# Optimization experiments

Measured on AMD Instinct MI355X. Metric: run time of the kernel, lower is better.

## Reference

```python
import jax, jax.numpy as jnp
import numpy as np

H = 256          # hidden_dim
B = 64           # molecules
M = 64           # atoms per molecule (equal-size molecules)
N = B * M        # total nodes
NE = 119         # element classes
NB = 5           # bond classes
EPS = 1e-5
OFF_I, OFF_J = np.where(~np.eye(M, dtype=bool))  # static off-diagonal pair order (i-major, j!=i)


def _gelu(x):
    return jax.nn.gelu(x, approximate=False)


def _ln(x, g, b):
    mu = jnp.mean(x, axis=-1, keepdims=True)
    var = jnp.mean((x - mu) ** 2, axis=-1, keepdims=True)
    return (x - mu) * jax.lax.rsqrt(var + EPS) * g + b


def _mlp(x, W1, b1, g, bn, W2, b2, W3, b3):
    x = _gelu(x @ W1 + b1)
    x = _ln(x, g, bn)
    x = _gelu(x @ W2 + b2)
    return x @ W3 + b3


def setup_inputs():
    key = jax.random.key(0)
    ks = jax.random.split(key, 16)
    s = 0.02
    def lin(k, fi, fo):
        return jax.random.normal(k, (fi, fo), jnp.float32) * s
    inp = {}
    inp["h"] = jax.random.normal(ks[0], (N, H), jnp.float32)
    inp["pos"] = jax.random.normal(ks[1], (N, 3), jnp.float32) * 3.0
    inp["edge_index"] = jax.random.randint(ks[2], (2, N * 8), 0, N)
    inp["batch"] = jnp.repeat(jnp.arange(B), M)
    # atom_predictor params
    inp["aW1"] = lin(ks[3], H, H); inp["ab1"] = jnp.zeros((H,))
    inp["ag"] = jnp.ones((H,)); inp["abn"] = jnp.zeros((H,))
    inp["aW2"] = lin(ks[4], H, H // 2); inp["ab2"] = jnp.zeros((H // 2,))
    inp["aW3"] = lin(ks[5], H // 2, NE); inp["ab3"] = jnp.zeros((NE,))
    # valency_predictor params
    inp["vW1"] = lin(ks[6], H + NE, H); inp["vb1"] = jnp.zeros((H,))
    inp["vg"] = jnp.ones((H,)); inp["vbn"] = jnp.zeros((H,))
    inp["vW2"] = lin(ks[7], H, H // 2); inp["vb2"] = jnp.zeros((H // 2,))
    inp["vW3"] = lin(ks[8], H // 2, 1); inp["vb3"] = jnp.zeros((1,))
    # bond_predictor params
    inp["bW1"] = lin(ks[9], 2 * H + 4, H); inp["bb1"] = jnp.zeros((H,))
    inp["bg"] = jnp.ones((H,)); inp["bbn"] = jnp.zeros((H,))
    inp["bW2"] = lin(ks[10], H, H // 2); inp["bb2"] = jnp.zeros((H // 2,))
    inp["bW3"] = lin(ks[11], H // 2, NB); inp["bb3"] = jnp.zeros((NB,))
    # chemical constant buffers (stand-ins for RDKit tables)
    mv = np.ones(NE, np.float32) * 4.0
    mv[[1, 9, 17, 35, 53]] = 1.0; mv[8] = 2.0; mv[7] = 3.0; mv[16] = 6.0; mv[15] = 5.0
    inp["max_valences"] = jnp.asarray(mv)
    cr = np.ones(NE, np.float32) * 1.5
    cr[1] = 0.31; cr[6] = 0.76; cr[7] = 0.71; cr[8] = 0.66; cr[9] = 0.57; cr[16] = 1.05
    inp["covalent_radii"] = jnp.asarray(cr)
    return inp


def _forward(h, pos, aW1, ab1, ag, abn, aW2, ab2, aW3, ab3,
             vW1, vb1, vg, vbn, vW2, vb2, vW3, vb3,
             bW1, bb1, bg, bbn, bW2, bb2, bW3, bb3,
             max_valences, covalent_radii):
    atom_logits = _mlp(h, aW1, ab1, ag, abn, aW2, ab2, aW3, ab3)        # [N,119]
    atom_probs = jax.nn.softmax(atom_logits, axis=-1)
    val = _mlp(jnp.concatenate([h, atom_probs], -1), vW1, vb1, vg, vbn, vW2, vb2, vW3, vb3)
    val = jax.nn.softplus(val)                                          # [N,1]
    pred = jnp.clip(jnp.argmax(atom_probs, -1), 0, 118)
    max_allowed = max_valences[pred]                                    # [N]
    # torch.min([N], [N,1]) broadcasts to [N,N] in the original -- reproduced faithfully
    valency_constrained = jnp.minimum(val[:, 0], max_allowed[:, None])  # [N,N]
    # vectorized pairwise bond prediction per molecule (equal-size molecules)
    hB = h.reshape(B, M, H)
    pB = pos.reshape(B, M, 3)
    probsB = atom_probs.reshape(B, M, NE)
    dist = jnp.linalg.norm(pB[:, :, None, :] - pB[:, None, :, :], axis=-1)  # [B,M,M]
    radii = covalent_radii[jnp.minimum(jnp.argmax(probsB, -1), 118)]        # [B,M]
    expected = radii[:, :, None] + radii[:, None, :]                        # [B,M,M]
    close = (dist < 3.0).astype(h.dtype)
    feats = jnp.concatenate([
        jnp.broadcast_to(hB[:, :, None, :], (B, M, M, H)),
        jnp.broadcast_to(hB[:, None, :, :], (B, M, M, H)),
        dist[..., None], expected[..., None],
        (dist / expected)[..., None], close[..., None],
    ], axis=-1)                                                             # [B,M,M,2H+4]
    logits = _mlp(feats, bW1, bb1, bg, bbn, bW2, bb2, bW3, bb3)             # [B,M,M,5]
    probs5 = jax.nn.softmax(logits, axis=-1)
    e0 = jnp.zeros((NB,), h.dtype).at[0].set(1.0)
    diag = jnp.eye(M, dtype=bool)[None, :, :, None]
    adjacency = jnp.where(diag, e0, probs5)                                 # [B,M,M,5]
    bond_logits = logits[:, OFF_I, OFF_J, :].reshape(B * M * (M - 1), NB)   # skip i==j, i-major order
    return (atom_logits, bond_logits, valency_constrained, adjacency)


def reference(h, pos, edge_index, batch, aW1, ab1, ag, abn, aW2, ab2, aW3, ab3,
              vW1, vb1, vg, vbn, vW2, vb2, vW3, vb3,
              bW1, bb1, bg, bbn, bW2, bb2, bW3, bb3, max_valences, covalent_radii):
    # edge_index is unused by the original forward; batch is implicit in the [B,M] layout
    return _forward(h, pos, aW1, ab1, ag, abn, aW2, ab2, aW3, ab3,
                    vW1, vb1, vg, vbn, vW2, vb2, vW3, vb3,
                    bW1, bb1, bg, bbn, bW2, bb2, bW3, bb3,
                    max_valences, covalent_radii)
```

## Files before the change

### kernel.cpp

```cpp
#include <hip/hip_runtime.h>
#include <math.h>

#define NN   4096
#define HH   256
#define NEC  119
#define NBC  5
#define NMOL 64
#define MAT  64

#define OFF_ATOM   0
#define SZ_ATOM    (4096*119)
#define OFF_BOND   487424
#define SZ_BOND    (258048*5)
#define OFF_VALM   (487424+1290240)
#define SZ_VALM    (4096*4096)
#define OFF_ADJ    (1777664+16777216)

typedef short  bf16x8 __attribute__((ext_vector_type(8)));
typedef float  f32x4  __attribute__((ext_vector_type(4)));

__device__ __forceinline__ float gelu_f(float x) {
    float z = fabsf(x) * 0.70710678118654752f;
    float t = __builtin_amdgcn_rcpf(fmaf(0.3275911f, z, 1.0f));
    float p = t * fmaf(t, fmaf(t, fmaf(t, fmaf(t, 1.061405429f, -1.453152027f),
                                       1.421413741f), -0.284496736f), 0.254829592f);
    float er = fmaf(-p, __expf(-z * z), 1.0f);
    float s = copysignf(er, x);
    return 0.5f * x * (1.f + s);
}
__device__ __forceinline__ unsigned short f2bf(float x) {
    unsigned int u = __float_as_uint(x);
    unsigned int r = (u + 0x7fffu + ((u >> 16) & 1u)) >> 16;
    return (unsigned short)r;
}

__global__ __launch_bounds__(256, 8) void k_front(
    const float* __restrict__ h,
    const float* __restrict__ aW1, const float* __restrict__ ab1,
    const float* __restrict__ ag,  const float* __restrict__ abn,
    const float* __restrict__ aW2, const float* __restrict__ ab2,
    const float* __restrict__ aW3, const float* __restrict__ ab3,
    const float* __restrict__ maxv, const float* __restrict__ covr,
    const float* __restrict__ vW1, const float* __restrict__ vb1,
    const float* __restrict__ vg,  const float* __restrict__ vbn,
    const float* __restrict__ vW2, const float* __restrict__ vb2,
    const float* __restrict__ vW3, const float* __restrict__ vb3,
    const float* __restrict__ bW1, const float* __restrict__ bb1,
    const float* __restrict__ bW2, const float* __restrict__ bW3,
    const float* __restrict__ bg,  const float* __restrict__ bbn,
    const float* __restrict__ bb2,
    float* __restrict__ logits_out,
    float* __restrict__ ma, float* __restrict__ rad, float* __restrict__ val,
    float* __restrict__ P, float* __restrict__ Q,
    short* __restrict__ W2f, short* __restrict__ W3f,
    float* __restrict__ uu, float* __restrict__ vvb)
{
    __shared__ float smem[3532];
    float (*hs)[376]   = (float(*)[376])smem;
    float (*z1)[256]   = (float(*)[256])(smem + 1504);
    float (*z2)[128]   = (float(*)[128])(smem + 2528);
    float (*llog)[120] = (float(*)[120])(smem + 3040);
    float (*redbuf)[2] = (float(*)[2])  (smem + 3520);

    const int t  = threadIdx.x;
    const int wv = t >> 6, ln = t & 63;

    if (blockIdx.x >= 1024) {
        const int pb = blockIdx.x - 1024;
        const int n0 = pb * 4;

        if (pb < 128) {
            const int id = pb * 256 + t;
            {
                const int e = id & 7, l = (id >> 3) & 63, ks = (id >> 9) & 7, ct = (id >> 12) & 7;
                const int k = ks * 32 + (l >> 4) * 8 + e;
                const int col = ct * 16 + (l & 15);
                W2f[id] = (short)f2bf(bW2[k * 128 + col]);
            }
            if (id < 2048) {
                const int e = id & 7, l = (id >> 3) & 63, ks = id >> 9;
                const int k = ks * 32 + (l >> 4) * 8 + e;
                const int col = l & 15;
                W3f[id] = (col < NBC) ? (short)f2bf(bW3[k * NBC + col]) : (short)0;
            }
        } else if (pb == 128) {
            if (t < 128) {
                float ua = 0.f, va = 0.f;
                for (int c = 0; c < 256; ++c) {
                    float w = bW2[c * 128 + t];
                    ua = fmaf(bg[c],  w, ua);
                    va = fmaf(bbn[c], w, va);
                }
                uu[t]  = ua;
                vvb[t] = va + bb2[t];
            }
        }

        float (*hq)[256] = (float(*)[256])smem;
        for (int idx = t; idx < 4 * 256; idx += 256)
            ((float*)hq)[idx] = h[(size_t)n0 * 256 + idx];
        __syncthreads();

        const int c = t;
        float accp[4], accq[4];
        float b1 = bb1[c];
        #pragma unroll
        for (int r = 0; r < 4; ++r) { accp[r] = b1; accq[r] = 0.f; }
        for (int k4 = 0; k4 < 64; ++k4) {
            const int k = k4 * 4;
            float p0 = bW1[(k + 0) * 256 + c];
            float p1 = bW1[(k + 1) * 256 + c];
            float p2 = bW1[(k + 2) * 256 + c];
            float p3 = bW1[(k + 3) * 256 + c];
            float q0 = bW1[(256 + k + 0) * 256 + c];
            float q1 = bW1[(256 + k + 1) * 256 + c];
            float q2 = bW1[(256 + k + 2) * 256 + c];
            float q3 = bW1[(256 + k + 3) * 256 + c];
            #pragma unroll
            for (int r = 0; r < 4; ++r) {
                float4 hv = *(const float4*)&hq[r][k];
                accp[r] = fmaf(hv.x, p0, accp[r]);
                accp[r] = fmaf(hv.y, p1, accp[r]);
                accp[r] = fmaf(hv.z, p2, accp[r]);
                accp[r] = fmaf(hv.w, p3, accp[r]);
                accq[r] = fmaf(hv.x, q0, accq[r]);
                accq[r] = fmaf(hv.y, q1, accq[r]);
                accq[r] = fmaf(hv.z, q2, accq[r]);
                accq[r] = fmaf(hv.w, q3, accq[r]);
            }
        }
        #pragma unroll
        for (int r = 0; r < 4; ++r) {
            P[(size_t)(n0 + r) * 256 + c] = accp[r];
            Q[(size_t)(n0 + r) * 256 + c] = accq[r];
        }
        return;
    }

    const int n0 = blockIdx.x * 4;

    for (int idx = t; idx < 4 * 256; idx += 256) {
        int r = idx >> 8, cc = idx & 255;
        hs[r][cc] = h[(size_t)(n0 + r) * 256 + cc];
    }
    if (t < 4) hs[t][375] = 0.f;
    __syncthreads();

    {
        const int c = t;
        float b1 = ab1[c];
        float acc[4];
        #pragma unroll
        for (int r = 0; r < 4; ++r) acc[r] = b1;
        for (int k4 = 0; k4 < 64; ++k4) {
            const int k = k4 * 4;
            float w0 = aW1[(k + 0) * 256 + c];
            float w1 = aW1[(k + 1) * 256 + c];
            float w2 = aW1[(k + 2) * 256 + c];
            float w3 = aW1[(k + 3) * 256 + c];
            #pragma unroll
            for (int r = 0; r < 4; ++r) {
                float4 hv = *(const float4*)&hs[r][k];
                acc[r] = fmaf(hv.x, w0, acc[r]);
                acc[r] = fmaf(hv.y, w1, acc[r]);
                acc[r] = fmaf(hv.z, w2, acc[r]);
                acc[r] = fmaf(hv.w, w3, acc[r]);
            }
        }
        #pragma unroll
        for (int r = 0; r < 4; ++r) z1[r][c] = gelu_f(acc[r]);
    }
    __syncthreads();

    {
        const int r = wv;
        float s = 0.f, s2 = 0.f;
        #pragma unroll
        for (int q = 0; q < 4; ++q) {
            float v = z1[r][ln + q * 64];
            s += v; s2 = fmaf(v, v, s2);
        }
        #pragma unroll
        for (int m = 32; m >= 1; m >>= 1) {
            s  += __shfl_xor(s,  m, 64);
            s2 += __shfl_xor(s2, m, 64);
        }
        if (ln == 0) {
            float mu  = s * (1.f / 256.f);
            float var = s2 * (1.f / 256.f) - mu * mu;
            redbuf[r][0] = mu;
            redbuf[r][1] = rsqrtf(var + 1e-5f);
        }
    }
    __syncthreads();
    {
        const int c = t;
        float g = ag[c], b = abn[c];
        #pragma unroll
        for (int r = 0; r < 4; ++r)
            z1[r][c] = (z1[r][c] - redbuf[r][0]) * redbuf[r][1] * g + b;
    }
    __syncthreads();

    {
        const int c2 = t & 127, kh = t >> 7;
        float acc2[4];
        #pragma unroll
        for (int r = 0; r < 4; ++r) acc2[r] = 0.f;
        const int kb = kh * 128;
        for (int k4 = 0; k4 < 32; ++k4) {
            const int k = kb + k4 * 4;
            float w0 = aW2[(k + 0) * 128 + c2];
            float w1 = aW2[(k + 1) * 128 + c2];
            float w2 = aW2[(k + 2) * 128 + c2];
            float w3 = aW2[(k + 3) * 128 + c2];
            #pragma unroll
            for (int r = 0; r < 4; ++r) {
                float4 zv = *(const float4*)&z1[r][k];
                acc2[r] = fmaf(zv.x, w0, acc2[r]);
                acc2[r] = fmaf(zv.y, w1, acc2[r]);
                acc2[r] = fmaf(zv.z, w2, acc2[r]);
                acc2[r] = fmaf(zv.w, w3, acc2[r]);
            }
        }
        if (kh == 1) {
            #pragma unroll
            for (int r = 0; r < 4; ++r) z2[r][c2] = acc2[r];
        }
        __syncthreads();
        if (kh == 0) {
            float b2 = ab2[c2];
            #pragma unroll
            for (int r = 0; r < 4; ++r)
                z2[r][c2] = gelu_f(acc2[r] + z2[r][c2] + b2);
        }
    }
    __syncthreads();

    if (t < NEC) {
        const int c = t;
        float b3 = ab3[c];
        float acc3[4];
        #pragma unroll
        for (int r = 0; r < 4; ++r) acc3[r] = b3;
        for (int k4 = 0; k4 < 32; ++k4) {
            const int k = k4 * 4;
            float w0 = aW3[(k + 0) * NEC + c];
            float w1 = aW3[(k + 1) * NEC + c];
            float w2 = aW3[(k + 2) * NEC + c];
            float w3 = aW3[(k + 3) * NEC + c];
            #pragma unroll
            for (int r = 0; r < 4; ++r) {
                float4 zv = *(const float4*)&z2[r][k];
                acc3[r] = fmaf(zv.x, w0, acc3[r]);
                acc3[r] = fmaf(zv.y, w1, acc3[r]);
                acc3[r] = fmaf(zv.z, w2, acc3[r]);
                acc3[r] = fmaf(zv.w, w3, acc3[r]);
            }
        }
        #pragma unroll
        for (int r = 0; r < 4; ++r) {
            llog[r][c] = acc3[r];
            logits_out[(size_t)(n0 + r) * NEC + c] = acc3[r];
        }
    }
    __syncthreads();

    {
        const int r = wv;
        float v1 = llog[r][ln];
        float v2 = (ln + 64 < NEC) ? llog[r][ln + 64] : -1e30f;
        float mx; int mi;
        if (v2 > v1) { mx = v2; mi = ln + 64; } else { mx = v1; mi = ln; }
        #pragma unroll
        for (int m = 32; m >= 1; m >>= 1) {
            float ov = __shfl_xor(mx, m, 64);
            int   oi = __shfl_xor(mi, m, 64);
            if (ov > mx || (ov == mx && oi < mi)) { mx = ov; mi = oi; }
        }
        float e1 = __expf(v1 - mx);
        float e2 = (ln + 64 < NEC) ? __expf(v2 - mx) : 0.f;
        float s = e1 + e2;
        #pragma unroll
        for (int m = 32; m >= 1; m >>= 1) s += __shfl_xor(s, m, 64);
        float inv = __builtin_amdgcn_rcpf(s);
        hs[r][256 + ln] = e1 * inv;
        if (ln + 64 < NEC) hs[r][256 + ln + 64] = e2 * inv;
        if (ln == 0) {
            ma[n0 + r]  = maxv[mi];
            rad[n0 + r] = covr[mi];
        }
    }
    __syncthreads();

    {
        const int c = t;
        float b1 = vb1[c];
        float acc[4];
        #pragma unroll
        for (int r = 0; r < 4; ++r) acc[r] = b1;
        for (int k4 = 0; k4 < 93; ++k4) {
            const int k = k4 * 4;
            float w0 = vW1[(k + 0) * 256 + c];
            float w1 = vW1[(k + 1) * 256 + c];
            float w2 = vW1[(k + 2) * 256 + c];
            float w3 = vW1[(k + 3) * 256 + c];
            #pragma unroll
            for (int r = 0; r < 4; ++r) {
                float4 hv = *(const float4*)&hs[r][k];
                acc[r] = fmaf(hv.x, w0, acc[r]);
                acc[r] = fmaf(hv.y, w1, acc[r]);
                acc[r] = fmaf(hv.z, w2, acc[r]);
                acc[r] = fmaf(hv.w, w3, acc[r]);
            }
        }
        {
            float w0 = vW1[372 * 256 + c];
            float w1 = vW1[373 * 256 + c];
            float w2 = vW1[374 * 256 + c];
            #pragma unroll
            for (int r = 0; r < 4; ++r) {
                acc[r] = fmaf(hs[r][372], w0, acc[r]);
                acc[r] = fmaf(hs[r][373], w1, acc[r]);
                acc[r] = fmaf(hs[r][374], w2, acc[r]);
            }
        }
        #pragma unroll
        for (int r = 0; r < 4; ++r) z1[r][c] = gelu_f(acc[r]);
    }
    __syncthreads();

    {
        const int r = wv;
        float s = 0.f, s2 = 0.f;
        #pragma unroll
        for (int q = 0; q < 4; ++q) {
            float v = z1[r][ln + q * 64];
            s += v; s2 = fmaf(v, v, s2);
        }
        #pragma unroll
        for (int m = 32; m >= 1; m >>= 1) {
            s  += __shfl_xor(s,  m, 64);
            s2 += __shfl_xor(s2, m, 64);
        }
        if (ln == 0) {
            float mu  = s * (1.f / 256.f);
            float var = s2 * (1.f / 256.f) - mu * mu;
            redbuf[r][0] = mu;
            redbuf[r][1] = rsqrtf(var + 1e-5f);
        }
    }
    __syncthreads();
    {
        const int c = t;
        float g = vg[c], b = vbn[c];
        #pragma unroll
        for (int r = 0; r < 4; ++r)
            z1[r][c] = (z1[r][c] - redbuf[r][0]) * redbuf[r][1] * g + b;
    }
    __syncthreads();

    {
        const int c2 = t & 127, kh = t >> 7;
        float acc2[4];
        #pragma unroll
        for (int r = 0; r < 4; ++r) acc2[r] = 0.f;
        const int kb = kh * 128;
        for (int k4 = 0; k4 < 32; ++k4) {
            const int k = kb + k4 * 4;
            float w0 = vW2[(k + 0) * 128 + c2];
            float w1 = vW2[(k + 1) * 128 + c2];
            float w2 = vW2[(k + 2) * 128 + c2];
            float w3 = vW2[(k + 3) * 128 + c2];
            #pragma unroll
            for (int r = 0; r < 4; ++r) {
                float4 zv = *(const float4*)&z1[r][k];
                acc2[r] = fmaf(zv.x, w0, acc2[r]);
                acc2[r] = fmaf(zv.y, w1, acc2[r]);
                acc2[r] = fmaf(zv.z, w2, acc2[r]);
                acc2[r] = fmaf(zv.w, w3, acc2[r]);
            }
        }
        if (kh == 1) {
            #pragma unroll
            for (int r = 0; r < 4; ++r) z2[r][c2] = acc2[r];
        }
        __syncthreads();
        if (kh == 0) {
            float b2 = vb2[c2];
            #pragma unroll
            for (int r = 0; r < 4; ++r)
                z2[r][c2] = gelu_f(acc2[r] + z2[r][c2] + b2);
        }
    }
    __syncthreads();

    {
        const int r = wv;
        float p = fmaf(z2[r][ln], vW3[ln], z2[r][ln + 64] * vW3[ln + 64]);
        #pragma unroll
        for (int m = 32; m >= 1; m >>= 1) p += __shfl_xor(p, m, 64);
        if (ln == 0) {
            float x = p + vb3[0];
            val[n0 + r] = (x > 15.f) ? x : log1pf(expf(x));
        }
    }
}

__global__ __launch_bounds__(256, 4) void k_back(
    const float* __restrict__ pos, const float* __restrict__ rad,
    const float* __restrict__ P, const float* __restrict__ Q,
    const float* __restrict__ bW1, const float* __restrict__ bg,
    const short* __restrict__ W2f, const short* __restrict__ W3f,
    const float* __restrict__ bb3,
    const float* __restrict__ uu, const float* __restrict__ vvb,
    const float* __restrict__ val, const float* __restrict__ ma,
    float* __restrict__ bond_logits, float* __restrict__ adjacency,
    float* __restrict__ valmat)
{
    __shared__ float posr[64][4];
    __shared__ float Pis[256];
    __shared__ float wst0[256], wst1[256], wst2[256], wst3[256];
    __shared__ float gams[256];
    __shared__ float us_[128], vbs[128];
    __shared__ unsigned short Ys[64 * 128];
    __shared__ float Ls[64][5];

    const int t  = threadIdx.x;

    if (blockIdx.x >= 4096) {
        const int i0 = (blockIdx.x - 4096) * 8;
        const float4* v4 = (const float4*)val;
        for (int rr = 0; rr < 8; ++rr) {
            const int i = i0 + rr;
            const float mi = ma[i];
            float4* o4 = (float4*)(valmat + (size_t)i * 4096);
            for (int j = t; j < 1024; j += 256) {
                float4 v = v4[j];
                float4 r;
                r.x = fminf(v.x, mi); r.y = fminf(v.y, mi);
                r.z = fminf(v.z, mi); r.w = fminf(v.w, mi);
                o4[j] = r;
            }
        }
        return;
    }

    const int bi = blockIdx.x;
    const int b  = bi >> 6, i = bi & 63;
    const int wv = t >> 6, ln = t & 63;
    const int lr = ln & 15, kg = ln >> 4;
    const int node0 = b * 64;
    const int j = wv * 16 + lr;

    if (t < 64) {
        int n = node0 + t;
        posr[t][0] = pos[n * 3 + 0];
        posr[t][1] = pos[n * 3 + 1];
        posr[t][2] = pos[n * 3 + 2];
        posr[t][3] = rad[n];
    }
    Pis[t]  = P[(size_t)(node0 + i) * 256 + t];
    wst0[t] = bW1[(size_t)512 * 256 + t];
    wst1[t] = bW1[(size_t)513 * 256 + t];
    wst2[t] = bW1[(size_t)514 * 256 + t];
    wst3[t] = bW1[(size_t)515 * 256 + t];
    gams[t] = bg[t];
    if (t < 128) { us_[t] = uu[t]; vbs[t] = vvb[t]; }
    __syncthreads();

    float dx = posr[i][0] - posr[j][0];
    float dy = posr[i][1] - posr[j][1];
    float dz = posr[i][2] - posr[j][2];
    float dist  = sqrtf(fmaf(dx, dx, fmaf(dy, dy, dz * dz)));
    float expd  = posr[i][3] + posr[j][3];
    float ratio = dist * __builtin_amdgcn_rcpf(expd);
    float close = (dist < 3.f) ? 1.f : 0.f;

    float s = 0.f, s2 = 0.f;
    bf16x8 afr[8];
    const float* Qrow = Q + (size_t)(node0 + j) * 256;
    #pragma unroll
    for (int ks = 0; ks < 8; ++ks) {
        const int base = ks * 32 + kg * 8;
        float4 Pa  = *(const float4*)&Pis[base],  Pb  = *(const float4*)&Pis[base + 4];
        float4 Qa  = *(const float4*)(Qrow + base), Qb = *(const float4*)(Qrow + base + 4);
        float4 w0a = *(const float4*)&wst0[base], w0b = *(const float4*)&wst0[base + 4];
        float4 w1a = *(const float4*)&wst1[base], w1b = *(const float4*)&wst1[base + 4];
        float4 w2a = *(const float4*)&wst2[base], w2b = *(const float4*)&wst2[base + 4];
        float4 w3a = *(const float4*)&wst3[base], w3b = *(const float4*)&wst3[base + 4];
        float4 ga  = *(const float4*)&gams[base], gb  = *(const float4*)&gams[base + 4];
        float g, xg;
        #define LANECH(P_, Q_, W0_, W1_, W2_, W3_, G_, EI) \
            g = P_ + Q_; g = fmaf(W0_, dist, g); g = fmaf(W1_, expd, g); \
            g = fmaf(W2_, ratio, g); g = fmaf(W3_, close, g); g = gelu_f(g); \
            s += g; s2 = fmaf(g, g, s2); xg = g * G_; afr[ks][EI] = (short)f2bf(xg);
        LANECH(Pa.x, Qa.x, w0a.x, w1a.x, w2a.x, w3a.x, ga.x, 0)
        LANECH(Pa.y, Qa.y, w0a.y, w1a.y, w2a.y, w3a.y, ga.y, 1)
        LANECH(Pa.z, Qa.z, w0a.z, w1a.z, w2a.z, w3a.z, ga.z, 2)
        LANECH(Pa.w, Qa.w, w0a.w, w1a.w, w2a.w, w3a.w, ga.w, 3)
        LANECH(Pb.x, Qb.x, w0b.x, w1b.x, w2b.x, w3b.x, gb.x, 4)
        LANECH(Pb.y, Qb.y, w0b.y, w1b.y, w2b.y, w3b.y, gb.y, 5)
        LANECH(Pb.z, Qb.z, w0b.z, w1b.z, w2b.z, w3b.z, gb.z, 6)
        LANECH(Pb.w, Qb.w, w0b.w, w1b.w, w2b.w, w3b.w, gb.w, 7)
        #undef LANECH
    }
    s  += __shfl_xor(s,  16, 64);  s  += __shfl_xor(s,  32, 64);
    s2 += __shfl_xor(s2, 16, 64);  s2 += __shfl_xor(s2, 32, 64);
    const float mu   = s * (1.f / 256.f);
    const float rstd = rsqrtf(s2 * (1.f / 256.f) - mu * mu + 1e-5f);

    f32x4 acc[8];
    #pragma unroll
    for (int ct = 0; ct < 8; ++ct) acc[ct] = (f32x4){0.f, 0.f, 0.f, 0.f};
    #pragma unroll
    for (int ks = 0; ks < 8; ++ks) {
        #pragma unroll
        for (int ct = 0; ct < 8; ++ct) {
            bf16x8 bfr = *(const bf16x8*)(W2f + (((size_t)(ct * 8 + ks)) * 64 + ln) * 8);
            acc[ct] = __builtin_amdgcn_mfma_f32_16x16x32_bf16(afr[ks], bfr, acc[ct], 0, 0, 0);
        }
    }

    float rst[4], rm[4];
    #pragma unroll
    for (int r = 0; r < 4; ++r) {
        float sr = __shfl(rstd, kg * 4 + r, 64);
        float mr = __shfl(mu,   kg * 4 + r, 64);
        rst[r] = sr; rm[r] = sr * mr;
    }
    #pragma unroll
    for (int ct = 0; ct < 8; ++ct) {
        const int col = ct * 16 + lr;
        const float ucv = us_[col], vcv = vbs[col];
        #pragma unroll
        for (int r = 0; r < 4; ++r) {
            float y = fmaf(rst[r], acc[ct][r], fmaf(-rm[r], ucv, vcv));
            y = gelu_f(y);
            const int row = wv * 16 + kg * 4 + r;
            const int chunk = col >> 3;
            const int off = row * 256 + ((chunk ^ (row & 7)) << 4) + ((col & 7) << 1);
            *(unsigned short*)((char*)Ys + off) = f2bf(y);
        }
    }

    {
        f32x4 acc3 = (f32x4){0.f, 0.f, 0.f, 0.f};
        #pragma unroll
        for (int ks = 0; ks < 4; ++ks) {
            bf16x8 bfr = *(const bf16x8*)(W3f + ((size_t)(ks * 64 + ln)) * 8);
            const int row   = wv * 16 + lr;
            const int chunk = ks * 4 + kg;
            const int off   = row * 256 + ((chunk ^ (row & 7)) << 4);
            bf16x8 afr2 = *(const bf16x8*)((char*)Ys + off);
            acc3 = __builtin_amdgcn_mfma_f32_16x16x32_bf16(afr2, bfr, acc3, 0, 0, 0);
        }
        if (lr < NBC) {
            #pragma unroll
            for (int r = 0; r < 4; ++r)
                Ls[wv * 16 + kg * 4 + r][lr] = acc3[r];
        }
    }

    const size_t adjbase  = (size_t)bi * 64 * 5;
    const size_t bondbase = ((size_t)b * 4032 + (size_t)i * 63) * 5;
    const float b30 = bb3[0], b31 = bb3[1], b32 = bb3[2], b33 = bb3[3], b34 = bb3[4];
    for (int u = ln; u < 80; u += 64) {
        const int jl = u / 5, o = u - jl * 5;
        const int j2 = wv * 16 + jl;
        float l0 = Ls[j2][0] + b30, l1 = Ls[j2][1] + b31, l2 = Ls[j2][2] + b32;
        float l3 = Ls[j2][3] + b33, l4 = Ls[j2][4] + b34;
        float mx = fmaxf(fmaxf(fmaxf(l0, l1), fmaxf(l2, l3)), l4);
        float e0 = __expf(l0 - mx), e1 = __expf(l1 - mx), e2 = __expf(l2 - mx);
        float e3 = __expf(l3 - mx), e4 = __expf(l4 - mx);
        float inv = __builtin_amdgcn_rcpf(e0 + e1 + e2 + e3 + e4);
        float lo = (o == 0) ? l0 : (o == 1) ? l1 : (o == 2) ? l2 : (o == 3) ? l3 : l4;
        float po = ((o == 0) ? e0 : (o == 1) ? e1 : (o == 2) ? e2 : (o == 3) ? e3 : e4) * inv;
        adjacency[adjbase + (size_t)j2 * 5 + o] = (j2 == i) ? ((o == 0) ? 1.f : 0.f) : po;
        if (j2 != i) {
            const int jj = j2 - (j2 > i ? 1 : 0);
            bond_logits[bondbase + (size_t)jj * 5 + o] = lo;
        }
    }
}

extern "C" void kernel_launch(void* const* d_in, const int* in_sizes, int n_in,
                              void* d_out, int out_size, void* d_ws, size_t ws_size,
                              hipStream_t stream)
{
    (void)in_sizes; (void)n_in; (void)out_size; (void)ws_size;
    const float* h   = (const float*)d_in[0];
    const float* pos = (const float*)d_in[1];
    const float* aW1 = (const float*)d_in[4];
    const float* ab1 = (const float*)d_in[5];
    const float* ag  = (const float*)d_in[6];
    const float* abn = (const float*)d_in[7];
    const float* aW2 = (const float*)d_in[8];
    const float* ab2 = (const float*)d_in[9];
    const float* aW3 = (const float*)d_in[10];
    const float* ab3 = (const float*)d_in[11];
    const float* vW1 = (const float*)d_in[12];
    const float* vb1 = (const float*)d_in[13];
    const float* vg  = (const float*)d_in[14];
    const float* vbn = (const float*)d_in[15];
    const float* vW2 = (const float*)d_in[16];
    const float* vb2 = (const float*)d_in[17];
    const float* vW3 = (const float*)d_in[18];
    const float* vb3 = (const float*)d_in[19];
    const float* bW1 = (const float*)d_in[20];
    const float* bb1 = (const float*)d_in[21];
    const float* bg  = (const float*)d_in[22];
    const float* bbn = (const float*)d_in[23];
    const float* bW2 = (const float*)d_in[24];
    const float* bb2 = (const float*)d_in[25];
    const float* bW3 = (const float*)d_in[26];
    const float* bb3 = (const float*)d_in[27];
    const float* mv  = (const float*)d_in[28];
    const float* cr  = (const float*)d_in[29];

    float* out = (float*)d_out;
    float* atom_logits = out + OFF_ATOM;
    float* bond_logits = out + OFF_BOND;
    float* valmat      = out + OFF_VALM;
    float* adjacency   = out + OFF_ADJ;

    float* ws    = (float*)d_ws;
    float* ma    = ws;
    float* rad   = ws + 4096;
    float* val   = ws + 8192;
    float* Pp    = ws + 12288;
    float* Qq    = ws + 1060864;
    short* W2f   = (short*)(ws + 2109440);
    short* W3f   = (short*)(ws + 2125824);
    float* uu    = ws + 2126848;
    float* vvb   = ws + 2126976;

    k_front<<<2048, 256, 0, stream>>>(h,
        aW1, ab1, ag, abn, aW2, ab2, aW3, ab3, mv, cr,
        vW1, vb1, vg, vbn, vW2, vb2, vW3, vb3,
        bW1, bb1, bW2, bW3, bg, bbn, bb2,
        atom_logits, ma, rad, val, Pp, Qq, W2f, W3f, uu, vvb);
    k_back<<<4608, 256, 0, stream>>>(pos, rad, Pp, Qq, bW1, bg,
                                     W2f, W3f, bb3, uu, vvb, val, ma,
                                     bond_logits, adjacency, valmat);
}
```

Measured before the change: 356.9 us.

## Move P/Q projection and valency MLP onto bf16 MFMA with a weight-prep kernel

Adds a k_prep kernel that converts the bond W1 (P/Q halves), valency W1/W2 and bond W2/W3 weights into bf16 MFMA fragment layouts. The front kernel now computes the P/Q node projections as 64x64 MFMA tiles and runs the valency MLP's first two layers with MFMA over swizzled bf16 LDS tiles. Row blocking for the atom MLP goes from 4 to 8 nodes per block, which halves the grid. Replacing scalar FP32 FMA loops with matrix instructions is meant to cut compute time, at the cost of bf16 rounding in these layers and one extra kernel launch.

```diff
diff --git a/kernel.cpp b/kernel.cpp
--- a/kernel.cpp
+++ b/kernel.cpp
@@ -5,15 +5,10 @@
 #define HH   256
 #define NEC  119
 #define NBC  5
-#define NMOL 64
-#define MAT  64
 
 #define OFF_ATOM   0
-#define SZ_ATOM    (4096*119)
 #define OFF_BOND   487424
-#define SZ_BOND    (258048*5)
 #define OFF_VALM   (487424+1290240)
-#define SZ_VALM    (4096*4096)
 #define OFF_ADJ    (1777664+16777216)
 
 typedef short  bf16x8 __attribute__((ext_vector_type(8)));
@@ -34,124 +29,171 @@
     return (unsigned short)r;
 }
 
-__global__ __launch_bounds__(256, 8) void k_front(
+__global__ __launch_bounds__(256) void k_prep(
+    const float* __restrict__ bW1, const float* __restrict__ bW2,
+    const float* __restrict__ bW3, const float* __restrict__ vW1,
+    const float* __restrict__ vW2,
+    const float* __restrict__ bg, const float* __restrict__ bbn,
+    const float* __restrict__ bb2,
+    short* __restrict__ PQf, short* __restrict__ V1f, short* __restrict__ V2vf,
+    short* __restrict__ W2f, short* __restrict__ W3f,
+    float* __restrict__ uu, float* __restrict__ vvb)
+{
+    const int t = threadIdx.x;
+    if (blockIdx.x == 1160) {
+        if (t < 128) {
+            float ua = 0.f, va = 0.f;
+            for (int c = 0; c < 256; ++c) {
+                float w = bW2[c * 128 + t];
+                ua = fmaf(bg[c],  w, ua);
+                va = fmaf(bbn[c], w, va);
+            }
+            uu[t]  = ua;
+            vvb[t] = va + bb2[t];
+        }
+        return;
+    }
+    const int id = blockIdx.x * 256 + t;
+    if (id < 131072) {
+        const int e = id & 7, l = (id >> 3) & 63;
+        const int rem = id >> 9, ks = rem & 7, ct = rem >> 3;
+        const int k = ks * 32 + (l >> 4) * 8 + e;
+        const int col = ct * 16 + (l & 15);
+        float v = (col < 256) ? bW1[k * 256 + col] : bW1[(256 + k) * 256 + (col - 256)];
+        PQf[id] = (short)f2bf(v);
+    } else if (id < 229376) {
+        const int id2 = id - 131072;
+        const int e = id2 & 7, l = (id2 >> 3) & 63;
+        const int rem = id2 >> 9, ks = rem % 12, ct = rem / 12;
+        const int kk = ks * 32 + (l >> 4) * 8 + e;
+        const int col = ct * 16 + (l & 15);
+        V1f[id2] = (kk < 375) ? (short)f2bf(vW1[kk * 256 + col]) : (short)0;
+    } else if (id < 262144) {
+        const int id3 = id - 229376;
+        const int e = id3 & 7, l = (id3 >> 3) & 63;
+        const int rem = id3 >> 9, ks = rem & 7, ct = rem >> 3;
+        const int k = ks * 32 + (l >> 4) * 8 + e;
+        const int col = ct * 16 + (l & 15);
+        V2vf[id3] = (short)f2bf(vW2[k * 128 + col]);
+    } else if (id < 294912) {
+        const int id4 = id - 262144;
+        const int e = id4 & 7, l = (id4 >> 3) & 63;
+        const int ks = (id4 >> 9) & 7, ct = (id4 >> 12) & 7;
+        const int k = ks * 32 + (l >> 4) * 8 + e;
+        const int col = ct * 16 + (l & 15);
+        W2f[id4] = (short)f2bf(bW2[k * 128 + col]);
+    } else if (id < 296960) {
+        const int id5 = id - 294912;
+        const int e = id5 & 7, l = (id5 >> 3) & 63, ks = id5 >> 9;
+        const int k = ks * 32 + (l >> 4) * 8 + e;
+        const int col = l & 15;
+        W3f[id5] = (col < NBC) ? (short)f2bf(bW3[k * NBC + col]) : (short)0;
+    }
+}
+
+__global__ __launch_bounds__(256, 3) void k_front(
     const float* __restrict__ h,
     const float* __restrict__ aW1, const float* __restrict__ ab1,
     const float* __restrict__ ag,  const float* __restrict__ abn,
     const float* __restrict__ aW2, const float* __restrict__ ab2,
     const float* __restrict__ aW3, const float* __restrict__ ab3,
     const float* __restrict__ maxv, const float* __restrict__ covr,
-    const float* __restrict__ vW1, const float* __restrict__ vb1,
-    const float* __restrict__ vg,  const float* __restrict__ vbn,
-    const float* __restrict__ vW2, const float* __restrict__ vb2,
+    const float* __restrict__ vb1, const float* __restrict__ vg,
+    const float* __restrict__ vbn, const float* __restrict__ vb2,
     const float* __restrict__ vW3, const float* __restrict__ vb3,
-    const float* __restrict__ bW1, const float* __restrict__ bb1,
-    const float* __restrict__ bW2, const float* __restrict__ bW3,
-    const float* __restrict__ bg,  const float* __restrict__ bbn,
-    const float* __restrict__ bb2,
+    const float* __restrict__ bb1,
+    const short* __restrict__ PQf, const short* __restrict__ V1f,
+    const short* __restrict__ V2vf,
     float* __restrict__ logits_out,
     float* __restrict__ ma, float* __restrict__ rad, float* __restrict__ val,
-    float* __restrict__ P, float* __restrict__ Q,
-    short* __restrict__ W2f, short* __restrict__ W3f,
-    float* __restrict__ uu, float* __restrict__ vvb)
+    float* __restrict__ P, float* __restrict__ Q)
 {
-    __shared__ float smem[3532];
-    float (*hs)[376]   = (float(*)[376])smem;
-    float (*z1)[256]   = (float(*)[256])(smem + 1504);
-    float (*z2)[128]   = (float(*)[128])(smem + 2528);
-    float (*llog)[120] = (float(*)[120])(smem + 3040);
-    float (*redbuf)[2] = (float(*)[2])  (smem + 3520);
+    __shared__ __align__(16) char smem[44864];
+    float (*hs)[256]   = (float(*)[256])(smem);
+    unsigned short* hb = (unsigned short*)(smem + 8192);
+    float (*z1)[256]   = (float(*)[256])(smem + 20480);
+    float (*z2)[128]   = (float(*)[128])(smem + 28672);
+    float (*llog)[120] = (float(*)[120])(smem + 32768);
+    unsigned short* zb = (unsigned short*)(smem + 36608);
+    float (*redbuf)[2] = (float(*)[2])(smem + 44800);
 
     const int t  = threadIdx.x;
     const int wv = t >> 6, ln = t & 63;
-
-    if (blockIdx.x >= 1024) {
-        const int pb = blockIdx.x - 1024;
-        const int n0 = pb * 4;
-
-        if (pb < 128) {
-            const int id = pb * 256 + t;
-            {
-                const int e = id & 7, l = (id >> 3) & 63, ks = (id >> 9) & 7, ct = (id >> 12) & 7;
-                const int k = ks * 32 + (l >> 4) * 8 + e;
-                const int col = ct * 16 + (l & 15);
-                W2f[id] = (short)f2bf(bW2[k * 128 + col]);
-            }
-            if (id < 2048) {
-                const int e = id & 7, l = (id >> 3) & 63, ks = id >> 9;
-                const int k = ks * 32 + (l >> 4) * 8 + e;
-                const int col = l & 15;
-                W3f[id] = (col < NBC) ? (short)f2bf(bW3[k * NBC + col]) : (short)0;
-            }
-        } else if (pb == 128) {
-            if (t < 128) {
-                float ua = 0.f, va = 0.f;
-                for (int c = 0; c < 256; ++c) {
-                    float w = bW2[c * 128 + t];
-                    ua = fmaf(bg[c],  w, ua);
-                    va = fmaf(bbn[c], w, va);
-                }
-                uu[t]  = ua;
-                vvb[t] = va + bb2[t];
-            }
-        }
-
-        float (*hq)[256] = (float(*)[256])smem;
-        for (int idx = t; idx < 4 * 256; idx += 256)
-            ((float*)hq)[idx] = h[(size_t)n0 * 256 + idx];
+    const int lr = ln & 15, kg = ln >> 4;
+
+    if (blockIdx.x >= 512) {
+        unsigned short* hbq = (unsigned short*)smem;
+        const int gb  = blockIdx.x - 512;
+        const int rt  = gb & 63, ct4 = gb >> 6;
+        const int n0  = rt * 64, c0 = ct4 * 64;
+
+        for (int i = 0; i < 16; ++i) {
+            const int idx4 = t + 256 * i;
+            const int r = idx4 >> 6, k4 = (idx4 & 63) * 4;
+            float4 hv = *(const float4*)(h + (size_t)(n0 + r) * 256 + k4);
+            ushort4 u;
+            u.x = f2bf(hv.x); u.y = f2bf(hv.y); u.z = f2bf(hv.z); u.w = f2bf(hv.w);
+            const int off = r * 512 + ((((k4 >> 3) ^ (r & 7))) << 4) + ((k4 & 7) << 1);
+            *(ushort4*)((char*)hbq + off) = u;
+        }
         __syncthreads();
 
-        const int c = t;
-        float accp[4], accq[4];
-        float b1 = bb1[c];
-        #pragma unroll
-        for (int r = 0; r < 4; ++r) { accp[r] = b1; accq[r] = 0.f; }
-        for (int k4 = 0; k4 < 64; ++k4) {
-            const int k = k4 * 4;
-            float p0 = bW1[(k + 0) * 256 + c];
-            float p1 = bW1[(k + 1) * 256 + c];
-            float p2 = bW1[(k + 2) * 256 + c];
-            float p3 = bW1[(k + 3) * 256 + c];
-            float q0 = bW1[(256 + k + 0) * 256 + c];
-            float q1 = bW1[(256 + k + 1) * 256 + c];
-            float q2 = bW1[(256 + k + 2) * 256 + c];
-            float q3 = bW1[(256 + k + 3) * 256 + c];
+        const int wr0 = wv * 16;
+        f32x4 acc[4];
+        #pragma unroll
+        for (int ctl = 0; ctl < 4; ++ctl) acc[ctl] = (f32x4){0.f, 0.f, 0.f, 0.f};
+        #pragma unroll
+        for (int ks = 0; ks < 8; ++ks) {
+            const int row = wr0 + lr;
+            const int chunk = ks * 4 + kg;
+            const int aoff = row * 512 + ((chunk ^ (row & 7)) << 4);
+            bf16x8 afr = *(const bf16x8*)((char*)hbq + aoff);
+            #pragma unroll
+            for (int ctl = 0; ctl < 4; ++ctl) {
+                const int ct_pq = ct4 * 4 + ctl;
+                bf16x8 bfr = *(const bf16x8*)(PQf + (((size_t)(ct_pq * 8 + ks)) * 64 + ln) * 8);
+                acc[ctl] = __builtin_amdgcn_mfma_f32_16x16x32_bf16(afr, bfr, acc[ctl], 0, 0, 0);
+            }
+        }
+        #pragma unroll
+        for (int ctl = 0; ctl < 4; ++ctl) {
+            const int colg = c0 + ctl * 16 + lr;
+            const float bias = (colg < 256) ? bb1[colg] : 0.f;
             #pragma unroll
             for (int r = 0; r < 4; ++r) {
-                float4 hv = *(const float4*)&hq[r][k];
-                accp[r] = fmaf(hv.x, p0, accp[r]);
-                accp[r] = fmaf(hv.y, p1, accp[r]);
-                accp[r] = fmaf(hv.z, p2, accp[r]);
-                accp[r] = fmaf(hv.w, p3, accp[r]);
-                accq[r] = fmaf(hv.x, q0, accq[r]);
-                accq[r] = fmaf(hv.y, q1, accq[r]);
-                accq[r] = fmaf(hv.z, q2, accq[r]);
-                accq[r] = fmaf(hv.w, q3, accq[r]);
-            }
-        }
-        #pragma unroll
-        for (int r = 0; r < 4; ++r) {
-            P[(size_t)(n0 + r) * 256 + c] = accp[r];
-            Q[(size_t)(n0 + r) * 256 + c] = accq[r];
+                const int n = n0 + wr0 + kg * 4 + r;
+                float v = acc[ctl][r] + bias;
+                if (colg < 256) P[(size_t)n * 256 + colg] = v;
+                else            Q[(size_t)n * 256 + (colg - 256)] = v;
+            }
         }
         return;
     }
 
-    const int n0 = blockIdx.x * 4;
-
-    for (int idx = t; idx < 4 * 256; idx += 256) {
-        int r = idx >> 8, cc = idx & 255;
-        hs[r][cc] = h[(size_t)(n0 + r) * 256 + cc];
-    }
-    if (t < 4) hs[t][375] = 0.f;
+    const int n0 = blockIdx.x * 8;
+
+    #pragma unroll
+    for (int i = 0; i < 3; ++i)
+        *(int4*)((char*)hb + (t + 256 * i) * 16) = (int4){0, 0, 0, 0};
+    *(int4*)((char*)zb + 4096 + t * 16) = (int4){0, 0, 0, 0};
+    for (int i = 0; i < 2; ++i) {
+        const int idx4 = t + 256 * i;
+        const int r = idx4 >> 6, k4 = (idx4 & 63) * 4;
+        float4 hv = *(const float4*)(h + (size_t)(n0 + r) * 256 + k4);
+        *(float4*)&hs[r][k4] = hv;
+        ushort4 u;
+        u.x = f2bf(hv.x); u.y = f2bf(hv.y); u.z = f2bf(hv.z); u.w = f2bf(hv.w);
+        const int off = r * 768 + ((((k4 >> 3) ^ (r & 7))) << 4) + ((k4 & 7) << 1);
+        *(ushort4*)((char*)hb + off) = u;
+    }
     __syncthreads();
 
     {
         const int c = t;
         float b1 = ab1[c];
-        float acc[4];
-        #pragma unroll
-        for (int r = 0; r < 4; ++r) acc[r] = b1;
+        float acc[8];
+        #pragma unroll
+        for (int r = 0; r < 8; ++r) acc[r] = b1;
         for (int k4 = 0; k4 < 64; ++k4) {
             const int k = k4 * 4;
             float w0 = aW1[(k + 0) * 256 + c];
@@ -159,7 +201,7 @@
             float w2 = aW1[(k + 2) * 256 + c];
             float w3 = aW1[(k + 3) * 256 + c];
             #pragma unroll
-            for (int r = 0; r < 4; ++r) {
+            for (int r = 0; r < 8; ++r) {
                 float4 hv = *(const float4*)&hs[r][k];
                 acc[r] = fmaf(hv.x, w0, acc[r]);
                 acc[r] = fmaf(hv.y, w1, acc[r]);
@@ -168,12 +210,12 @@
             }
         }
         #pragma unroll
-        for (int r = 0; r < 4; ++r) z1[r][c] = gelu_f(acc[r]);
-    }
-    __syncthreads();
-
-    {
-        const int r = wv;
+        for (int r = 0; r < 8; ++r) z1[r][c] = gelu_f(acc[r]);
+    }
+    __syncthreads();
+
+    for (int rr = 0; rr < 2; ++rr) {
+        const int r = wv * 2 + rr;
         float s = 0.f, s2 = 0.f;
         #pragma unroll
         for (int q = 0; q < 4; ++q) {
@@ -197,16 +239,16 @@
         const int c = t;
         float g = ag[c], b = abn[c];
         #pragma unroll
-        for (int r = 0; r < 4; ++r)
+        for (int r = 0; r < 8; ++r)
             z1[r][c] = (z1[r][c] - redbuf[r][0]) * redbuf[r][1] * g + b;
     }
     __syncthreads();
 
     {
         const int c2 = t & 127, kh = t >> 7;
-        float acc2[4];
-        #pragma unroll
-        for (int r = 0; r < 4; ++r) acc2[r] = 0.f;
+        float acc2[8];
+        #pragma unroll
+        for (int r = 0; r < 8; ++r) acc2[r] = 0.f;
         const int kb = kh * 128;
         for (int k4 = 0; k4 < 32; ++k4) {
             const int k = kb + k4 * 4;
@@ -215,7 +257,7 @@
             float w2 = aW2[(k + 2) * 128 + c2];
             float w3 = aW2[(k + 3) * 128 + c2];
             #pragma unroll
-            for (int r = 0; r < 4; ++r) {
+            for (int r = 0; r < 8; ++r) {
                 float4 zv = *(const float4*)&z1[r][k];
                 acc2[r] = fmaf(zv.x, w0, acc2[r]);
                 acc2[r] = fmaf(zv.y, w1, acc2[r]);
@@ -225,13 +267,13 @@
         }
         if (kh == 1) {
             #pragma unroll
-            for (int r = 0; r < 4; ++r) z2[r][c2] = acc2[r];
+            for (int r = 0; r < 8; ++r) z2[r][c2] = acc2[r];
         }
         __syncthreads();
         if (kh == 0) {
             float b2 = ab2[c2];
             #pragma unroll
-            for (int r = 0; r < 4; ++r)
+            for (int r = 0; r < 8; ++r)
                 z2[r][c2] = gelu_f(acc2[r] + z2[r][c2] + b2);
         }
     }
@@ -240,9 +282,9 @@
     if (t < NEC) {
         const int c = t;
         float b3 = ab3[c];
-        float acc3[4];
-        #pragma unroll
-        for (int r = 0; r < 4; ++r) acc3[r] = b3;
+        float acc3[8];
+        #pragma unroll
+        for (int r = 0; r < 8; ++r) acc3[r] = b3;
         for (int k4 = 0; k4 < 32; ++k4) {
             const int k = k4 * 4;
             float w0 = aW3[(k + 0) * NEC + c];
@@ -250,7 +292,7 @@
             float w2 = aW3[(k + 2) * NEC + c];
             float w3 = aW3[(k + 3) * NEC + c];
             #pragma unroll
-            for (int r = 0; r < 4; ++r) {
+            for (int r = 0; r < 8; ++r) {
                 float4 zv = *(const float4*)&z2[r][k];
                 acc3[r] = fmaf(zv.x, w0, acc3[r]);
                 acc3[r] = fmaf(zv.y, w1, acc3[r]);
@@ -259,15 +301,15 @@
             }
         }
         #pragma unroll
-        for (int r = 0; r < 4; ++r) {
+        for (int r = 0; r < 8; ++r) {
             llog[r][c] = acc3[r];
             logits_out[(size_t)(n0 + r) * NEC + c] = acc3[r];
         }
     }
     __syncthreads();
 
-    {
-        const int r = wv;
+    for (int rr = 0; rr < 2; ++rr) {
+        const int r = wv * 2 + rr;
         float v1 = llog[r][ln];
         float v2 = (ln + 64 < NEC) ? llog[r][ln + 64] : -1e30f;
         float mx; int mi;
@@ -284,8 +326,16 @@
         #pragma unroll
         for (int m = 32; m >= 1; m >>= 1) s += __shfl_xor(s, m, 64);
         float inv = __builtin_amdgcn_rcpf(s);
-        hs[r][256 + ln] = e1 * inv;
-        if (ln + 64 < NEC) hs[r][256 + ln + 64] = e2 * inv;
+        {
+            const int cf = 256 + ln;
+            const int off = r * 768 + ((((cf >> 3) ^ (r & 7))) << 4) + ((cf & 7) << 1);
+            *(unsigned short*)((char*)hb + off) = f2bf(e1 * inv);
+        }
+        if (ln + 64 < NEC) {
+            const int cf = 256 + ln + 64;
+            const int off = r * 768 + ((((cf >> 3) ^ (r & 7))) << 4) + ((cf & 7) << 1);
+            *(unsigned short*)((char*)hb + off) = f2bf(e2 * inv);
+        }
         if (ln == 0) {
             ma[n0 + r]  = maxv[mi];
             rad[n0 + r] = covr[mi];
@@ -294,44 +344,37 @@
     __syncthreads();
 
     {
-        const int c = t;
-        float b1 = vb1[c];
-        float acc[4];
-        #pragma unroll
-        for (int r = 0; r < 4; ++r) acc[r] = b1;
-        for (int k4 = 0; k4 < 93; ++k4) {
-            const int k = k4 * 4;
-            float w0 = vW1[(k + 0) * 256 + c];
-            float w1 = vW1[(k + 1) * 256 + c];
-            float w2 = vW1[(k + 2) * 256 + c];
-            float w3 = vW1[(k + 3) * 256 + c];
-            #pragma unroll
-            for (int r = 0; r < 4; ++r) {
-                float4 hv = *(const float4*)&hs[r][k];
-                acc[r] = fmaf(hv.x, w0, acc[r]);
-                acc[r] = fmaf(hv.y, w1, acc[r]);
-                acc[r] = fmaf(hv.z, w2, acc[r]);
-                acc[r] = fmaf(hv.w, w3, acc[r]);
-            }
-        }
-        {
-            float w0 = vW1[372 * 256 + c];
-            float w1 = vW1[373 * 256 + c];
-            float w2 = vW1[374 * 256 + c];
-            #pragma unroll
-            for (int r = 0; r < 4; ++r) {
-                acc[r] = fmaf(hs[r][372], w0, acc[r]);
-                acc[r] = fmaf(hs[r][373], w1, acc[r]);
-                acc[r] = fmaf(hs[r][374], w2, acc[r]);
-            }
-        }
-        #pragma unroll
-        for (int r = 0; r < 4; ++r) z1[r][c] = gelu_f(acc[r]);
-    }
-    __syncthreads();
-
-    {
-        const int r = wv;
+        f32x4 acc[4];
+        #pragma unroll
+        for (int ctl = 0; ctl < 4; ++ctl) acc[ctl] = (f32x4){0.f, 0.f, 0.f, 0.f};
+        #pragma unroll
+        for (int ks = 0; ks < 12; ++ks) {
+            const int row = lr;
+            const int chunk = ks * 4 + kg;
+            const int aoff = row * 768 + ((chunk ^ (row & 7)) << 4);
+            bf16x8 afr = *(const bf16x8*)((char*)hb + aoff);
+            #pragma unroll
+            for (int ctl = 0; ctl < 4; ++ctl) {
+                const int ctg = wv * 4 + ctl;
+                bf16x8 bfr = *(const bf16x8*)(V1f + (((size_t)(ctg * 12 + ks)) * 64 + ln) * 8);
+                acc[ctl] = __builtin_amdgcn_mfma_f32_16x16x32_bf16(afr, bfr, acc[ctl], 0, 0, 0);
+            }
+        }
+        if (kg < 2) {
+            #pragma unroll
+            for (int ctl = 0; ctl < 4; ++ctl) {
+                const int col = (wv * 4 + ctl) * 16 + lr;
+                const float b1 = vb1[col];
+                #pragma unroll
+                for (int r = 0; r < 4; ++r)
+                    z1[kg * 4 + r][col] = gelu_f(acc[ctl][r] + b1);
+            }
+        }
+    }
+    __syncthreads();
+
+    for (int rr = 0; rr < 2; ++rr) {
+        const int r = wv * 2 + rr;
         float s = 0.f, s2 = 0.f;
         #pragma unroll
         for (int q = 0; q < 4; ++q) {
@@ -355,48 +398,46 @@
         const int c = t;
         float g = vg[c], b = vbn[c];
         #pragma unroll
-        for (int r = 0; r < 4; ++r)
-            z1[r][c] = (z1[r][c] - redbuf[r][0]) * redbuf[r][1] * g + b;
+        for (int r = 0; r < 8; ++r) {
+            float v = (z1[r][c] - redbuf[r][0]) * redbuf[r][1] * g + b;
+            const int off = r * 512 + ((((c >> 3) ^ (r & 7))) << 4) + ((c & 7) << 1);
+            *(unsigned short*)((char*)zb + off) = f2bf(v);
+        }
     }
     __syncthreads();
 
     {
-        const int c2 = t & 127, kh = t >> 7;
-        float acc2[4];
-        #pragma unroll
-        for (int r = 0; r < 4; ++r) acc2[r] = 0.f;
-        const int kb = kh * 128;
-        for (int k4 = 0; k4 < 32; ++k4) {
-            const int k = kb + k4 * 4;
-            float w0 = vW2[(k + 0) * 128 + c2];
-            float w1 = vW2[(k + 1) * 128 + c2];
-            float w2 = vW2[(k + 2) * 128 + c2];
-            float w3 = vW2[(k + 3) * 128 + c2];
-            #pragma unroll
-            for (int r = 0; r < 4; ++r) {
-                float4 zv = *(const float4*)&z1[r][k];
-                acc2[r] = fmaf(zv.x, w0, acc2[r]);
-                acc2[r] = fmaf(zv.y, w1, acc2[r]);
-                acc2[r] = fmaf(zv.z, w2, acc2[r]);
-                acc2[r] = fmaf(zv.w, w3, acc2[r]);
-            }
-        }
-        if (kh == 1) {
-            #pragma unroll
-            for (int r = 0; r < 4; ++r) z2[r][c2] = acc2[r];
-        }
-        __syncthreads();
-        if (kh == 0) {
-            float b2 = vb2[c2];
-            #pragma unroll
-            for (int r = 0; r < 4; ++r)
-                z2[r][c2] = gelu_f(acc2[r] + z2[r][c2] + b2);
-        }
-    }
-    __syncthreads();
-
-    {
-        const int r = wv;
+        f32x4 acc2[2];
+        #pragma unroll
+        for (int c2 = 0; c2 < 2; ++c2) acc2[c2] = (f32x4){0.f, 0.f, 0.f, 0.f};
+        #pragma unroll
+        for (int ks = 0; ks < 8; ++ks) {
+            const int row = lr;
+            const int chunk = ks * 4 + kg;
+            const int aoff = row * 512 + ((chunk ^ (row & 7)) << 4);
+            bf16x8 afr = *(const bf16x8*)((char*)zb + aoff);
+            #pragma unroll
+            for (int c2 = 0; c2 < 2; ++c2) {
+                const int ctg = wv * 2 + c2;
+                bf16x8 bfr = *(const bf16x8*)(V2vf + (((size_t)(ctg * 8 + ks)) * 64 + ln) * 8);
+                acc2[c2] = __builtin_amdgcn_mfma_f32_16x16x32_bf16(afr, bfr, acc2[c2], 0, 0, 0);
+            }
+        }
+        if (kg < 2) {
+            #pragma unroll
+            for (int c2 = 0; c2 < 2; ++c2) {
+                const int col = (wv * 2 + c2) * 16 + lr;
+                const float b2 = vb2[col];
+                #pragma unroll
+                for (int r = 0; r < 4; ++r)
+                    z2[kg * 4 + r][col] = gelu_f(acc2[c2][r] + b2);
+            }
+        }
+    }
+    __syncthreads();
+
+    for (int rr = 0; rr < 2; ++rr) {
+        const int r = wv * 2 + rr;
         float p = fmaf(z2[r][ln], vW3[ln], z2[r][ln + 64] * vW3[ln + 64]);
         #pragma unroll
         for (int m = 32; m >= 1; m >>= 1) p += __shfl_xor(p, m, 64);
@@ -630,16 +671,21 @@
     float* val   = ws + 8192;
     float* Pp    = ws + 12288;
     float* Qq    = ws + 1060864;
-    short* W2f   = (short*)(ws + 2109440);
-    short* W3f   = (short*)(ws + 2125824);
-    float* uu    = ws + 2126848;
-    float* vvb   = ws + 2126976;
-
-    k_front<<<2048, 256, 0, stream>>>(h,
+    float* uu    = ws + 2109440;
+    float* vvb   = ws + 2109568;
+    short* W2f   = (short*)(ws + 2109696);
+    short* W3f   = (short*)(ws + 2126080);
+    short* PQf   = (short*)(ws + 2127104);
+    short* V1f   = (short*)(ws + 2192640);
+    short* V2vf  = (short*)(ws + 2241792);
+
+    k_prep<<<1161, 256, 0, stream>>>(bW1, bW2, bW3, vW1, vW2, bg, bbn, bb2,
+                                     PQf, V1f, V2vf, W2f, W3f, uu, vvb);
+    k_front<<<1024, 256, 0, stream>>>(h,
         aW1, ab1, ag, abn, aW2, ab2, aW3, ab3, mv, cr,
-        vW1, vb1, vg, vbn, vW2, vb2, vW3, vb3,
-        bW1, bb1, bW2, bW3, bg, bbn, bb2,
-        atom_logits, ma, rad, val, Pp, Qq, W2f, W3f, uu, vvb);
+        vb1, vg, vbn, vb2, vW3, vb3, bb1,
+        PQf, V1f, V2vf,
+        atom_logits, ma, rad, val, Pp, Qq);
     k_back<<<4608, 256, 0, stream>>>(pos, rad, Pp, Qq, bW1, bg,
                                      W2f, W3f, bb3, uu, vvb, val, ma,
                                      bond_logits, adjacency, valmat);
```

Result: faster. 299.4 us (-16.1%).
